# Optimization experiments

Measured on AMD Instinct MI355X. Metric: run time of the kernel, lower is better.

## Reference

```python
import jax, jax.numpy as jnp
import numpy as np

B, N, S, K, CIN = 16, 4096, 1024, 32, 64
EPS = 1e-5


def setup_inputs() -> dict:
    key = jax.random.key(0)
    ks = jax.random.split(key, 6)
    xyz = jax.random.normal(ks[0], (B, N, 3), jnp.float32)
    features = jax.random.normal(ks[1], (B, N, CIN), jnp.float32)
    # random sampling without replacement (mirrors torch.randperm(N)[:npoint])
    fps_idx = jax.vmap(lambda k: jax.random.permutation(k, N)[:S])(
        jax.random.split(ks[2], B)).astype(jnp.int32)
    chans = [CIN + 3, 64, 64, 128]
    params = {}
    for i in range(3):
        cin, cout = chans[i], chans[i + 1]
        params[f"W{i}"] = jax.random.normal(ks[3 + i], (cout, cin), jnp.float32) / np.sqrt(cin).astype(np.float32)
        params[f"b{i}"] = jnp.zeros((cout,), jnp.float32)
        params[f"g{i}"] = jnp.ones((cout,), jnp.float32)
        params[f"bt{i}"] = jnp.zeros((cout,), jnp.float32)
    return dict(xyz=xyz, features=features, fps_idx=fps_idx, **params)


def _mlp_layer(x, W, b, g, bt):
    # x: (B*S, Cin, K); Conv1d(kernel=1) + BatchNorm1d (training stats) + ReLU
    y = jnp.einsum('oc,bck->bok', W, x) + b[None, :, None]
    mu = y.mean(axis=(0, 2), keepdims=True)
    var = y.var(axis=(0, 2), keepdims=True)  # biased var, as in BN normalization
    y = (y - mu) * jax.lax.rsqrt(var + EPS) * g[None, :, None] + bt[None, :, None]
    return jax.nn.relu(y)


def reference(xyz, features, fps_idx, W0, b0, g0, bt0, W1, b1, g1, bt1, W2, b2, g2, bt2):
    # sample centers: (B, S, 3)
    new_xyz = jnp.take_along_axis(xyz, fps_idx[..., None], axis=1)
    # squared pairwise distances (B, S, N)
    d = (jnp.sum(new_xyz * new_xyz, -1)[..., None]
         + jnp.sum(xyz * xyz, -1)[:, None, :]
         - 2.0 * jnp.einsum('bsd,bnd->bsn', new_xyz, xyz))
    _, idx = jax.lax.top_k(-d, K)  # k nearest -> (B, S, K)
    bidx = jnp.arange(B)[:, None, None]
    g_xyz = xyz[bidx, idx] - new_xyz[:, :, None, :]  # (B, S, K, 3) relative coords
    g_feat = features[bidx, idx]                     # (B, S, K, CIN)
    grouped = jnp.concatenate([g_xyz, g_feat], axis=-1)  # (B, S, K, CIN+3)
    x = grouped.reshape(B * S, K, CIN + 3).transpose(0, 2, 1)  # (B*S, C, K)
    x = _mlp_layer(x, W0, b0, g0, bt0)
    x = _mlp_layer(x, W1, b1, g1, bt1)
    x = _mlp_layer(x, W2, b2, g2, bt2)
    new_features = x.max(axis=-1).reshape(B, S, -1)  # (B, S, 128)
    return new_xyz, new_features
```

## Files before the change

kernel.cpp:

```cpp
#include <hip/hip_runtime.h>
#include <stdint.h>

#define B_   16
#define N_   4096
#define S_   1024
#define K_   32
#define CIN_ 64
#define P_   524288
#define PQ_  16384
#define EPS_ 1e-5f

#define SZ_IDX    ((size_t)P_ * 4)
#define SZ_Y      ((size_t)P_ * 64 * 2)
#define SZ_MX     ((size_t)PQ_ * 128 * 4)
#define OFF_IDX   ((size_t)0)
#define OFF_Y0    (OFF_IDX + SZ_IDX)
#define OFF_Y1    (OFF_Y0 + SZ_Y)
#define OFF_MX    (OFF_Y1 + SZ_Y)
#define OFF_MN    (OFF_MX + SZ_MX)
#define OFF_STATS (OFF_MN + SZ_MX)
#define OFF_FIN   (OFF_STATS + 16384)
#define OFF_FPSC  (OFF_FIN + 2048)
#define OFF_PXYZW (OFF_FPSC + (size_t)PQ_ * 4)
#define WS_NEEDED (OFF_PXYZW + (size_t)B_ * N_ * 16)

typedef unsigned short u16;
typedef short bfrag __attribute__((ext_vector_type(8)));
typedef float f32x4 __attribute__((ext_vector_type(4)));

__device__ __forceinline__ float b2f(unsigned v) {
  return __uint_as_float((v & 0xffffu) << 16);
}
__device__ __forceinline__ u16 f2b(float f) {
  unsigned u = __float_as_uint(f);
  unsigned r = (u + 0x7fffu + ((u >> 16) & 1u)) >> 16;
  return (u16)r;
}
__device__ __forceinline__ unsigned pk2(float a, float b) {
  return (unsigned)f2b(a) | ((unsigned)f2b(b) << 16);
}

__global__ __launch_bounds__(256) void fps_canon_kernel(
    const int* __restrict__ fpsraw, int* __restrict__ fpsc)
{
  __shared__ int is64;
  const int tid = threadIdx.x;
  if (tid == 0) is64 = 1;
  __syncthreads();
  if (tid < 64) {
    if (fpsraw[2 * tid + 1] != 0) atomicAnd(&is64, 0);
  }
  __syncthreads();
  int i = blockIdx.x * 256 + tid;
  if (i < PQ_) {
    int src = is64 ? (2 * i) : i;
    int v = fpsraw[src];
    fpsc[i] = (v & 0xFFF);
  }
}

__global__ __launch_bounds__(256) void prep_kernel(
    const float* __restrict__ xyz, float4* __restrict__ pxyzw)
{
  int i = blockIdx.x * 256 + threadIdx.x;
  float x0 = xyz[i*3+0], x1 = xyz[i*3+1], x2 = xyz[i*3+2];
  float s2 = __fadd_rn(__fadd_rn(__fmul_rn(x0,x0), __fmul_rn(x1,x1)), __fmul_rn(x2,x2));
  pxyzw[i] = make_float4(x0, x1, x2, s2);
}

#define NBIN 2048
#define CAND_CAP 512

__global__ __launch_bounds__(256) void knn_kernel(
    const float4* __restrict__ pxyzw, const int* __restrict__ fps,
    int* __restrict__ idxout, float* __restrict__ out_xyz)
{
  __shared__ unsigned hist[NBIN];
  __shared__ float cd[CAND_CAP];
  __shared__ int   ci_[CAND_CAP];
  __shared__ int   sel[K_];
  __shared__ int   sCnt, sCand, sT;

  const int q   = blockIdx.x;
  const int b   = q >> 10;
  const int tid = threadIdx.x;
  const float4* xb4 = pxyzw + (size_t)b * N_;
  const int ctr = fps[q];
  const float4 cv = xb4[ctr];
  const float cx = cv.x, cy = cv.y, cz = cv.z, s1 = cv.w;

  if (tid == 0) {
    out_xyz[(size_t)q*3+0] = cx;
    out_xyz[(size_t)q*3+1] = cy;
    out_xyz[(size_t)q*3+2] = cz;
    sCnt = 0; sCand = 0;
  }
  {
    uint4* hz = (uint4*)hist;
    hz[tid]       = make_uint4(0,0,0,0);
    hz[tid + 256] = make_uint4(0,0,0,0);
  }
  __syncthreads();

  float dreg[16];
  unsigned bpk[8];
  #pragma unroll
  for (int it = 0; it < 16; ++it) {
    int n = it * 256 + tid;
    float4 v = xb4[n];
    float dt = __fadd_rn(__fadd_rn(__fmul_rn(cx,v.x), __fmul_rn(cy,v.y)), __fmul_rn(cz,v.z));
    float d  = __fsub_rn(__fadd_rn(s1, v.w), __fmul_rn(2.0f, dt));
    dreg[it] = d;
    int bin = (int)(d * 128.0f);
    bin = bin > (NBIN-1) ? (NBIN-1) : bin;
    bin = bin < 0 ? 0 : bin;
    if (it & 1) bpk[it >> 1] |= (unsigned)bin << 16;
    else        bpk[it >> 1]  = (unsigned)bin;
    atomicAdd(&hist[bin], 1u);
  }
  __syncthreads();

  const int lane = tid & 63, wid = tid >> 6;
  if (wid == 0) {
    int cum = 0, base = 0, found = 0;
    while (!found && base < NBIN) {
      int h = (int)hist[base + lane];
      int pre = h;
      #pragma unroll
      for (int off = 1; off < 64; off <<= 1) {
        int v = __shfl_up(pre, off, 64);
        if (lane >= off) pre += v;
      }
      int tot = __shfl(pre, 63, 64);
      bool cross = (cum + pre >= K_) && (cum + pre - h < K_);
      unsigned long long mm = __ballot(cross);
      if (mm) {
        if (lane == 0) sT = base + (int)(__ffsll((long long)mm) - 1);
        found = 1;
      }
      cum += tot;
      base += 64;
    }
  }
  __syncthreads();
  const int T = sT;

  #pragma unroll
  for (int it = 0; it < 16; ++it) {
    int bin = (int)((bpk[it >> 1] >> ((it & 1) * 16)) & 0xFFFFu);
    if (bin <= T) {
      int n = it * 256 + tid;
      if (bin < T) {
        int s = atomicAdd(&sCnt, 1);
        if (s < K_) sel[s] = n;
      } else {
        int s = atomicAdd(&sCand, 1);
        if (s < CAND_CAP) { cd[s] = dreg[it]; ci_[s] = n; }
      }
    }
  }
  __syncthreads();

  if (wid == 0) {
    int m = sCnt; m = m > K_ ? K_ : m;
    int cc = sCand; cc = cc > CAND_CAP ? CAND_CAP : cc;
    const int r = K_ - m;
    for (int it = 0; it < r; ++it) {
      float bd = 3.0e38f; int bi = 0x7fffffff;
      for (int j = lane; j < cc; j += 64) {
        float dv = cd[j]; int iv = ci_[j];
        if (dv < bd || (dv == bd && iv < bi)) { bd = dv; bi = iv; }
      }
      #pragma unroll
      for (int off = 32; off > 0; off >>= 1) {
        float od = __shfl_down(bd, off, 64);
        int   oi = __shfl_down(bi, off, 64);
        if (od < bd || (od == bd && oi < bi)) { bd = od; bi = oi; }
      }
      int win = __shfl(bi, 0, 64);
      if (lane == 0) sel[m + it] = win & 0xFFF;
      for (int j = lane; j < cc; j += 64) if (ci_[j] == win) cd[j] = 3.0e38f;
    }
  }
  __syncthreads();
  if (tid < K_) idxout[(size_t)q * K_ + tid] = sel[tid] & 0xFFF;
}


__global__ __launch_bounds__(256) void l0_mfma(
    const float* __restrict__ xyz, const float* __restrict__ feat,
    const int* __restrict__ fps, const int* __restrict__ idxin,
    const float* __restrict__ W0, const float* __restrict__ b0,
    uint4* __restrict__ Y0g, float* __restrict__ sumg, float* __restrict__ sqg)
{
  __shared__ uint4 Wl[12*64];
  __shared__ float bl[64];
  __shared__ float ssum[64], ssq[64];

  const int tid = threadIdx.x;
  const int bid0 = blockIdx.x;
  const int rep = (bid0 & 7) << 9;
  const int bid = (bid0 & 7) * ((int)gridDim.x >> 3) + (bid0 >> 3);
  const int pbase = bid * 128;
  const int q0 = bid * 4;
  const int b = bid >> 8;

  if (tid < 64) { bl[tid] = b0 ? b0[tid] : 0.f; ssum[tid] = 0.f; ssq[tid] = 0.f; }
  for (int u = tid; u < 12*64; u += 256) {
    int kc = u >> 6, o = u & 63;
    unsigned pk[4];
    #pragma unroll
    for (int hh = 0; hh < 4; ++hh) {
      int c0 = kc*8 + hh*2, c1 = c0 + 1;
      float v0 = (c0 < 64) ? W0[o*67 + 3 + c0] : (c0 < 67 ? W0[o*67 + (c0-64)] : 0.f);
      float v1 = (c1 < 64) ? W0[o*67 + 3 + c1] : (c1 < 67 ? W0[o*67 + (c1-64)] : 0.f);
      pk[hh] = pk2(v0, v1);
    }
    Wl[u] = make_uint4(pk[0], pk[1], pk[2], pk[3]);
  }

  const int lane = tid & 63, w = tid >> 6, g = lane >> 4, fr = lane & 15;
  const float* xb = xyz + (size_t)b * N_ * 3;
  const float* fbase = feat + (size_t)b * N_ * 64;

  int pidx[2];
  const int ct = fps[q0 + w] & 0xFFF;
  #pragma unroll
  for (int pm = 0; pm < 2; ++pm)
    pidx[pm] = idxin[pbase + w*32 + pm*16 + fr] & 0xFFF;

  bfrag xv[3][2];
  #pragma unroll
  for (int kk = 0; kk < 3; ++kk) {
    const int kc = kk*4 + g;
    #pragma unroll
    for (int pm = 0; pm < 2; ++pm) {
      uint4 uu;
      if (kc < 8) {
        const float* fp = fbase + pidx[pm]*64 + kc*8;
        float4 fa = *(const float4*)fp;
        float4 fb2 = *(const float4*)(fp + 4);
        uu = make_uint4(pk2(fa.x, fa.y), pk2(fa.z, fa.w),
                        pk2(fb2.x, fb2.y), pk2(fb2.z, fb2.w));
      } else if (kc == 8) {
        int n = pidx[pm];
        float dx = xb[n*3+0] - xb[ct*3+0];
        float dy = xb[n*3+1] - xb[ct*3+1];
        float dz = xb[n*3+2] - xb[ct*3+2];
        uu = make_uint4(pk2(dx, dy), (unsigned)f2b(dz), 0u, 0u);
      } else {
        uu = make_uint4(0u, 0u, 0u, 0u);
      }
      xv[kk][pm] = *(bfrag*)&uu;
    }
  }
  __syncthreads();

  f32x4 acc[4][2];
  #pragma unroll
  for (int m = 0; m < 4; ++m)
    #pragma unroll
    for (int j = 0; j < 4; ++j) {
      float v = bl[m*16 + g*4 + j];
      acc[m][0][j] = v; acc[m][1][j] = v;
    }
  #pragma unroll
  for (int kk = 0; kk < 3; ++kk) {
    const int kc = kk*4 + g;
    bfrag a[4];
    #pragma unroll
    for (int m = 0; m < 4; ++m) { uint4 u = Wl[kc*64 + m*16 + fr]; a[m] = *(bfrag*)&u; }
    #pragma unroll
    for (int m = 0; m < 4; ++m)
      #pragma unroll
      for (int pm = 0; pm < 2; ++pm)
        acc[m][pm] = __builtin_amdgcn_mfma_f32_16x16x32_bf16(a[m], xv[kk][pm], acc[m][pm], 0, 0, 0);
  }

  #pragma unroll
  for (int m = 0; m < 4; ++m) {
    #pragma unroll
    for (int j = 0; j < 4; ++j) {
      float v0 = acc[m][0][j], v1 = acc[m][1][j];
      float s = v0 + v1, s2 = v0*v0 + v1*v1;
      #pragma unroll
      for (int d = 1; d < 16; d <<= 1) { s += __shfl_xor(s, d); s2 += __shfl_xor(s2, d); }
      if (fr == 0) {
        atomicAdd(&ssum[m*16 + g*4 + j], s);
        atomicAdd(&ssq[m*16 + g*4 + j], s2);
      }
    }
    #pragma unroll
    for (int pm = 0; pm < 2; ++pm) {
      unsigned lo = pk2(acc[m][pm][0], acc[m][pm][1]);
      unsigned hi = pk2(acc[m][pm][2], acc[m][pm][3]);
      unsigned plo = (unsigned)__shfl_xor((int)lo, 16, 64);
      unsigned phi = (unsigned)__shfl_xor((int)hi, 16, 64);
      if ((g & 1) == 0) {
        size_t unit = (size_t)(m*2 + (g>>1)) * P_ + pbase + w*32 + pm*16 + fr;
        Y0g[unit] = make_uint4(lo, hi, plo, phi);
      }
    }
  }
  __syncthreads();
  if (tid < 64) { atomicAdd(&sumg[rep + tid], ssum[tid]); atomicAdd(&sqg[rep + tid], ssq[tid]); }
}

__global__ __launch_bounds__(256) void l1_mfma(
    const uint4* __restrict__ Y0g,
    const float* __restrict__ W1, const float* __restrict__ b1,
    const float* __restrict__ sc0, const float* __restrict__ sh0,
    uint4* __restrict__ Y1g, float* __restrict__ sumg, float* __restrict__ sqg)
{
  __shared__ uint4 Wl[8*64];
  __shared__ float scl[64], shl[64], bl[64];
  __shared__ float ssum[64], ssq[64];

  const int tid = threadIdx.x;
  const int bid0 = blockIdx.x;
  const int rep = (bid0 & 7) << 9;
  const int bid = (bid0 & 7) * ((int)gridDim.x >> 3) + (bid0 >> 3);
  const int pbase = bid * 128;

  if (tid < 64) {
    scl[tid] = sc0[tid]; shl[tid] = sh0[tid];
    bl[tid] = b1 ? b1[tid] : 0.f;
    ssum[tid] = 0.f; ssq[tid] = 0.f;
  }
  for (int u = tid; u < 8*64; u += 256) {
    int kc = u >> 6, o = u & 63;
    const float* wp = W1 + o*64 + kc*8;
    float4 wa = *(const float4*)wp;
    float4 wb = *(const float4*)(wp + 4);
    Wl[u] = make_uint4(pk2(wa.x, wa.y), pk2(wa.z, wa.w), pk2(wb.x, wb.y), pk2(wb.z, wb.w));
  }
  __syncthreads();

  const int lane = tid & 63, w = tid >> 6, g = lane >> 4, fr = lane & 15;

  bfrag xv[2][2];
  #pragma unroll
  for (int kk = 0; kk < 2; ++kk) {
    const int kc = kk*4 + g;
    float4 sa = *(const float4*)&scl[kc*8];
    float4 sb = *(const float4*)&scl[kc*8 + 4];
    float4 ha = *(const float4*)&shl[kc*8];
    float4 hb = *(const float4*)&shl[kc*8 + 4];
    #pragma unroll
    for (int pm = 0; pm < 2; ++pm) {
      uint4 yv = Y0g[(size_t)kc * P_ + pbase + w*32 + pm*16 + fr];
      unsigned r0 = pk2(fmaxf(fmaf(sa.x, b2f(yv.x),       ha.x), 0.f),
                        fmaxf(fmaf(sa.y, b2f(yv.x >> 16), ha.y), 0.f));
      unsigned r1 = pk2(fmaxf(fmaf(sa.z, b2f(yv.y),       ha.z), 0.f),
                        fmaxf(fmaf(sa.w, b2f(yv.y >> 16), ha.w), 0.f));
      unsigned r2 = pk2(fmaxf(fmaf(sb.x, b2f(yv.z),       hb.x), 0.f),
                        fmaxf(fmaf(sb.y, b2f(yv.z >> 16), hb.y), 0.f));
      unsigned r3 = pk2(fmaxf(fmaf(sb.z, b2f(yv.w),       hb.z), 0.f),
                        fmaxf(fmaf(sb.w, b2f(yv.w >> 16), hb.w), 0.f));
      uint4 uu = make_uint4(r0, r1, r2, r3);
      xv[kk][pm] = *(bfrag*)&uu;
    }
  }

  f32x4 acc[4][2];
  #pragma unroll
  for (int m = 0; m < 4; ++m)
    #pragma unroll
    for (int j = 0; j < 4; ++j) {
      float v = bl[m*16 + g*4 + j];
      acc[m][0][j] = v; acc[m][1][j] = v;
    }
  #pragma unroll
  for (int kk = 0; kk < 2; ++kk) {
    const int kc = kk*4 + g;
    bfrag a[4];
    #pragma unroll
    for (int m = 0; m < 4; ++m) { uint4 u = Wl[kc*64 + m*16 + fr]; a[m] = *(bfrag*)&u; }
    #pragma unroll
    for (int m = 0; m < 4; ++m)
      #pragma unroll
      for (int pm = 0; pm < 2; ++pm)
        acc[m][pm] = __builtin_amdgcn_mfma_f32_16x16x32_bf16(a[m], xv[kk][pm], acc[m][pm], 0, 0, 0);
  }

  #pragma unroll
  for (int m = 0; m < 4; ++m) {
    #pragma unroll
    for (int j = 0; j < 4; ++j) {
      float v0 = acc[m][0][j], v1 = acc[m][1][j];
      float s = v0 + v1, s2 = v0*v0 + v1*v1;
      #pragma unroll
      for (int d = 1; d < 16; d <<= 1) { s += __shfl_xor(s, d); s2 += __shfl_xor(s2, d); }
      if (fr == 0) {
        atomicAdd(&ssum[m*16 + g*4 + j], s);
        atomicAdd(&ssq[m*16 + g*4 + j], s2);
      }
    }
    #pragma unroll
    for (int pm = 0; pm < 2; ++pm) {
      unsigned lo = pk2(acc[m][pm][0], acc[m][pm][1]);
      unsigned hi = pk2(acc[m][pm][2], acc[m][pm][3]);
      unsigned plo = (unsigned)__shfl_xor((int)lo, 16, 64);
      unsigned phi = (unsigned)__shfl_xor((int)hi, 16, 64);
      if ((g & 1) == 0) {
        size_t unit = (size_t)(m*2 + (g>>1)) * P_ + pbase + w*32 + pm*16 + fr;
        Y1g[unit] = make_uint4(lo, hi, plo, phi);
      }
    }
  }
  __syncthreads();
  if (tid < 64) { atomicAdd(&sumg[rep + tid], ssum[tid]); atomicAdd(&sqg[rep + tid], ssq[tid]); }
}

__global__ __launch_bounds__(256) void l2_mfma(
    const uint4* __restrict__ Y1g,
    const float* __restrict__ W2, const float* __restrict__ b2,
    const float* __restrict__ sc1, const float* __restrict__ sh1,
    float* __restrict__ mxg, float* __restrict__ mng,
    float* __restrict__ sumg, float* __restrict__ sqg)
{
  __shared__ uint4 Wl[8*128];
  __shared__ float scl[64], shl[64], bl[128];
  __shared__ float ssum[128], ssq[128];

  const int tid = threadIdx.x;
  const int bid0 = blockIdx.x;
  const int rep = (bid0 & 7) << 9;
  const int bid = (bid0 & 7) * ((int)gridDim.x >> 3) + (bid0 >> 3);
  const int pbase = bid * 128;
  const int q0 = bid * 4;

  if (tid < 64) { scl[tid] = sc1[tid]; shl[tid] = sh1[tid]; }
  if (tid < 128) { bl[tid] = b2 ? b2[tid] : 0.f; ssum[tid] = 0.f; ssq[tid] = 0.f; }
  for (int u = tid; u < 8*128; u += 256) {
    int kc = u >> 7, o = u & 127;
    const float* wp = W2 + o*64 + kc*8;
    float4 wa = *(const float4*)wp;
    float4 wb = *(const float4*)(wp + 4);
    Wl[u] = make_uint4(pk2(wa.x, wa.y), pk2(wa.z, wa.w), pk2(wb.x, wb.y), pk2(wb.z, wb.w));
  }
  __syncthreads();

  const int lane = tid & 63, w = tid >> 6, g = lane >> 4, fr = lane & 15;

  bfrag ax[2][2];
  #pragma unroll
  for (int kk = 0; kk < 2; ++kk) {
    const int kc = kk*4 + g;
    float4 sa = *(const float4*)&scl[kc*8];
    float4 sb = *(const float4*)&scl[kc*8 + 4];
    float4 ha = *(const float4*)&shl[kc*8];
    float4 hb = *(const float4*)&shl[kc*8 + 4];
    #pragma unroll
    for (int pm = 0; pm < 2; ++pm) {
      uint4 yv = Y1g[(size_t)kc * P_ + pbase + w*32 + pm*16 + fr];
      unsigned r0 = pk2(fmaxf(fmaf(sa.x, b2f(yv.x),       ha.x), 0.f),
                        fmaxf(fmaf(sa.y, b2f(yv.x >> 16), ha.y), 0.f));
      unsigned r1 = pk2(fmaxf(fmaf(sa.z, b2f(yv.y),       ha.z), 0.f),
                        fmaxf(fmaf(sa.w, b2f(yv.y >> 16), ha.w), 0.f));
      unsigned r2 = pk2(fmaxf(fmaf(sb.x, b2f(yv.z),       hb.x), 0.f),
                        fmaxf(fmaf(sb.y, b2f(yv.z >> 16), hb.y), 0.f));
      unsigned r3 = pk2(fmaxf(fmaf(sb.z, b2f(yv.w),       hb.z), 0.f),
                        fmaxf(fmaf(sb.w, b2f(yv.w >> 16), hb.w), 0.f));
      uint4 uu = make_uint4(r0, r1, r2, r3);
      ax[kk][pm] = *(bfrag*)&uu;
    }
  }

  f32x4 acc[2][8];
  #pragma unroll
  for (int cn = 0; cn < 8; ++cn) {
    float v = bl[cn*16 + fr];
    #pragma unroll
    for (int j = 0; j < 4; ++j) { acc[0][cn][j] = v; acc[1][cn][j] = v; }
  }
  #pragma unroll
  for (int kk = 0; kk < 2; ++kk) {
    const int kc = kk*4 + g;
    #pragma unroll
    for (int cn = 0; cn < 8; ++cn) {
      uint4 u = Wl[kc*128 + cn*16 + fr];
      bfrag bw = *(bfrag*)&u;
      acc[0][cn] = __builtin_amdgcn_mfma_f32_16x16x32_bf16(ax[kk][0], bw, acc[0][cn], 0, 0, 0);
      acc[1][cn] = __builtin_amdgcn_mfma_f32_16x16x32_bf16(ax[kk][1], bw, acc[1][cn], 0, 0, 0);
    }
  }

  #pragma unroll
  for (int cn = 0; cn < 8; ++cn) {
    float mx = -3.0e38f, mn = 3.0e38f, s = 0.f, s2 = 0.f;
    #pragma unroll
    for (int pm = 0; pm < 2; ++pm)
      #pragma unroll
      for (int j = 0; j < 4; ++j) {
        float v = acc[pm][cn][j];
        mx = fmaxf(mx, v); mn = fminf(mn, v);
        s += v; s2 += v*v;
      }
    #pragma unroll
    for (int d = 16; d < 64; d <<= 1) {
      mx = fmaxf(mx, __shfl_xor(mx, d));
      mn = fminf(mn, __shfl_xor(mn, d));
      s  += __shfl_xor(s, d);
      s2 += __shfl_xor(s2, d);
    }
    if (g == 0) {
      int o = cn*16 + fr;
      size_t q = q0 + w;
      mxg[q*128 + o] = mx;
      mng[q*128 + o] = mn;
      atomicAdd(&ssum[o], s);
      atomicAdd(&ssq[o], s2);
    }
  }
  __syncthreads();
  if (tid < 128) { atomicAdd(&sumg[rep + tid], ssum[tid]); atomicAdd(&sqg[rep + tid], ssq[tid]); }
}

__global__ void finalize_kernel(
    const float* __restrict__ sum, const float* __restrict__ sq,
    const float* __restrict__ g, const float* __restrict__ bt,
    float* __restrict__ sc, float* __restrict__ sh, int C)
{
  int c = threadIdx.x;
  if (c < C) {
    float s = 0.f, s2 = 0.f;
    #pragma unroll
    for (int r = 0; r < 8; ++r) { s += sum[r*512 + c]; s2 += sq[r*512 + c]; }
    const float inv = 1.0f / (float)P_;
    float mu = s * inv;
    float var = s2 * inv - mu * mu;
    var = fmaxf(var, 0.f);
    float rr = 1.0f / sqrtf(var + EPS_);
    float gg = g ? g[c] : 1.0f;
    float bb = bt ? bt[c] : 0.0f;
    float sv = gg * rr;
    sc[c] = sv;
    sh[c] = bb - mu * sv;
  }
}

__global__ __launch_bounds__(256) void out_kernel(
    const float* __restrict__ mxg, const float* __restrict__ mng,
    const float* __restrict__ sc2, const float* __restrict__ sh2,
    float* __restrict__ out)
{
  int i = blockIdx.x * 256 + threadIdx.x;
  int o = i & 127;
  float a = sc2[o];
  float v = (a >= 0.f) ? mxg[i] : mng[i];
  float z = fmaxf(fmaf(a, v, sh2[o]), 0.f);
  out[(size_t)PQ_ * 3 + i] = z;
}

extern "C" void kernel_launch(void* const* d_in, const int* in_sizes, int n_in,
                              void* d_out, int out_size, void* d_ws, size_t ws_size,
                              hipStream_t stream)
{
  int i_xyz=-1, i_feat=-1, i_fps=-1, i_w0=-1, i_w1=-1, i_w2=-1;
  for (int i = 0; i < n_in; ++i) {
    switch (in_sizes[i]) {
      case 196608:  i_xyz = i; break;
      case 4194304: i_feat = i; break;
      case 16384:   i_fps = i; break;
      case 4288:    i_w0 = i; break;
      case 4096:    i_w1 = i; break;
      case 8192:    i_w2 = i; break;
      default: break;
    }
  }
  if (i_xyz < 0 || i_feat < 0 || i_fps < 0 || i_w0 < 0 || i_w1 < 0 || i_w2 < 0) return;

  const float* xyz  = (const float*)d_in[i_xyz];
  const float* feat = (const float*)d_in[i_feat];
  const int*   fpsr = (const int*)d_in[i_fps];
  const float* W0 = (const float*)d_in[i_w0];
  const float* W1 = (const float*)d_in[i_w1];
  const float* W2 = (const float*)d_in[i_w2];

  bool canon = (n_in >= 15 && i_xyz==0 && i_feat==1 && i_fps==2 && i_w0==3 &&
                i_w1==7 && i_w2==11 &&
                in_sizes[4]==64 && in_sizes[5]==64 && in_sizes[6]==64 &&
                in_sizes[8]==64 && in_sizes[9]==64 && in_sizes[10]==64 &&
                in_sizes[12]==128 && in_sizes[13]==128 && in_sizes[14]==128);
  const float* b0 = canon ? (const float*)d_in[4]  : nullptr;
  const float* g0 = canon ? (const float*)d_in[5]  : nullptr;
  const float* bt0= canon ? (const float*)d_in[6]  : nullptr;
  const float* b1 = canon ? (const float*)d_in[8]  : nullptr;
  const float* g1 = canon ? (const float*)d_in[9]  : nullptr;
  const float* bt1= canon ? (const float*)d_in[10] : nullptr;
  const float* b2 = canon ? (const float*)d_in[12] : nullptr;
  const float* g2 = canon ? (const float*)d_in[13] : nullptr;
  const float* bt2= canon ? (const float*)d_in[14] : nullptr;

  float* out = (float*)d_out;
  char* ws = (char*)d_ws;
  if (ws_size < WS_NEEDED) return;

  int* idxw = (int*)(ws + OFF_IDX);
  uint4* Y0 = (uint4*)(ws + OFF_Y0);
  uint4* Y1 = (uint4*)(ws + OFF_Y1);
  float* mxg = (float*)(ws + OFF_MX);
  float* mng = (float*)(ws + OFF_MN);
  float* st  = (float*)(ws + OFF_STATS);
  float* fin = (float*)(ws + OFF_FIN);
  int* fpsc  = (int*)(ws + OFF_FPSC);
  float4* pxyzw = (float4*)(ws + OFF_PXYZW);

  hipMemsetAsync(st, 0, 16384, stream);

  fps_canon_kernel<<<(PQ_+255)/256, 256, 0, stream>>>(fpsr, fpsc);
  prep_kernel<<<(B_*N_)/256, 256, 0, stream>>>(xyz, pxyzw);

  knn_kernel<<<PQ_, 256, 0, stream>>>(pxyzw, fpsc, idxw, out);

  l0_mfma<<<P_/128, 256, 0, stream>>>(xyz, feat, fpsc, idxw, W0, b0, Y0, st + 0, st + 64);
  finalize_kernel<<<1, 64, 0, stream>>>(st + 0, st + 64, g0, bt0, fin + 0, fin + 64, 64);

  l1_mfma<<<P_/128, 256, 0, stream>>>(Y0, W1, b1, fin + 0, fin + 64, Y1, st + 128, st + 192);
  finalize_kernel<<<1, 64, 0, stream>>>(st + 128, st + 192, g1, bt1, fin + 128, fin + 192, 64);

  l2_mfma<<<P_/128, 256, 0, stream>>>(Y1, W2, b2, fin + 128, fin + 192, mxg, mng, st + 256, st + 384);
  finalize_kernel<<<1, 128, 0, stream>>>(st + 256, st + 384, g2, bt2, fin + 256, fin + 384, 128);

  out_kernel<<<(PQ_*128)/256, 256, 0, stream>>>(mxg, mng, fin + 256, fin + 384, out);
}
```

Baseline: 238.4 us.

## Process two kNN queries per block with packed 16-bit histograms

Each kNN block now handles two query centers, so every loaded point coordinate is reused for two distance computations. The two histograms are packed as 16-bit halves of 32-bit words to keep shared memory the same size. Distances are recomputed for boundary candidates instead of being held in registers, and two wavefronts do the threshold scan and selection in parallel. The aim is to halve point loads and block count. The costs are more register pressure and possible atomic contention on the packed counters; a bin count over 65535 would overflow, though with 4096 points per query this cannot happen.

```diff
diff --git a/kernel.cpp b/kernel.cpp
--- a/kernel.cpp
+++ b/kernel.cpp
@@ -75,56 +75,62 @@
     const float4* __restrict__ pxyzw, const int* __restrict__ fps,
     int* __restrict__ idxout, float* __restrict__ out_xyz)
 {
-  __shared__ unsigned hist[NBIN];
-  __shared__ float cd[CAND_CAP];
-  __shared__ int   ci_[CAND_CAP];
-  __shared__ int   sel[K_];
-  __shared__ int   sCnt, sCand, sT;
-
-  const int q   = blockIdx.x;
-  const int b   = q >> 10;
+  __shared__ unsigned histp[2][NBIN/2];
+  __shared__ float cd[2][CAND_CAP];
+  __shared__ int   ci_[2][CAND_CAP];
+  __shared__ int   sel[2][K_];
+  __shared__ int   sCnt[2], sCand[2], sT[2];
+
+  const int q0  = blockIdx.x * 2;
+  const int b   = q0 >> 10;
   const int tid = threadIdx.x;
   const float4* xb4 = pxyzw + (size_t)b * N_;
-  const int ctr = fps[q];
-  const float4 cv = xb4[ctr];
-  const float cx = cv.x, cy = cv.y, cz = cv.z, s1 = cv.w;
-
-  if (tid == 0) {
-    out_xyz[(size_t)q*3+0] = cx;
-    out_xyz[(size_t)q*3+1] = cy;
-    out_xyz[(size_t)q*3+2] = cz;
-    sCnt = 0; sCand = 0;
+  const int ctr0 = fps[q0]     & 0xFFF;
+  const int ctr1 = fps[q0 + 1] & 0xFFF;
+  const float4 c0 = xb4[ctr0];
+  const float4 c1 = xb4[ctr1];
+
+  if (tid < 2) {
+    const float4 cc = tid ? c1 : c0;
+    out_xyz[(size_t)(q0 + tid)*3+0] = cc.x;
+    out_xyz[(size_t)(q0 + tid)*3+1] = cc.y;
+    out_xyz[(size_t)(q0 + tid)*3+2] = cc.z;
+    sCnt[tid] = 0; sCand[tid] = 0;
   }
   {
-    uint4* hz = (uint4*)hist;
-    hz[tid]       = make_uint4(0,0,0,0);
+    uint4* hz = (uint4*)&histp[0][0];
+    hz[tid] = make_uint4(0,0,0,0);
     hz[tid + 256] = make_uint4(0,0,0,0);
   }
   __syncthreads();
 
-  float dreg[16];
-  unsigned bpk[8];
+  unsigned bpk0[8], bpk1[8];
   #pragma unroll
   for (int it = 0; it < 16; ++it) {
     int n = it * 256 + tid;
     float4 v = xb4[n];
-    float dt = __fadd_rn(__fadd_rn(__fmul_rn(cx,v.x), __fmul_rn(cy,v.y)), __fmul_rn(cz,v.z));
-    float d  = __fsub_rn(__fadd_rn(s1, v.w), __fmul_rn(2.0f, dt));
-    dreg[it] = d;
-    int bin = (int)(d * 128.0f);
-    bin = bin > (NBIN-1) ? (NBIN-1) : bin;
-    bin = bin < 0 ? 0 : bin;
-    if (it & 1) bpk[it >> 1] |= (unsigned)bin << 16;
-    else        bpk[it >> 1]  = (unsigned)bin;
-    atomicAdd(&hist[bin], 1u);
+    float dt0 = __fadd_rn(__fadd_rn(__fmul_rn(c0.x,v.x), __fmul_rn(c0.y,v.y)), __fmul_rn(c0.z,v.z));
+    float d0  = __fsub_rn(__fadd_rn(c0.w, v.w), __fmul_rn(2.0f, dt0));
+    float dt1 = __fadd_rn(__fadd_rn(__fmul_rn(c1.x,v.x), __fmul_rn(c1.y,v.y)), __fmul_rn(c1.z,v.z));
+    float d1  = __fsub_rn(__fadd_rn(c1.w, v.w), __fmul_rn(2.0f, dt1));
+    int b0 = (int)(d0 * 128.0f);
+    b0 = b0 > (NBIN-1) ? (NBIN-1) : b0; b0 = b0 < 0 ? 0 : b0;
+    int b1 = (int)(d1 * 128.0f);
+    b1 = b1 > (NBIN-1) ? (NBIN-1) : b1; b1 = b1 < 0 ? 0 : b1;
+    if (it & 1) { bpk0[it >> 1] |= (unsigned)b0 << 16; bpk1[it >> 1] |= (unsigned)b1 << 16; }
+    else        { bpk0[it >> 1]  = (unsigned)b0;       bpk1[it >> 1]  = (unsigned)b1; }
+    atomicAdd(&histp[0][b0 >> 1], (b0 & 1) ? 0x10000u : 1u);
+    atomicAdd(&histp[1][b1 >> 1], (b1 & 1) ? 0x10000u : 1u);
   }
   __syncthreads();
 
   const int lane = tid & 63, wid = tid >> 6;
-  if (wid == 0) {
+  if (wid < 2) {
+    const unsigned* hq = &histp[wid][0];
     int cum = 0, base = 0, found = 0;
     while (!found && base < NBIN) {
-      int h = (int)hist[base + lane];
+      int bn = base + lane;
+      int h = (int)((hq[bn >> 1] >> ((bn & 1) * 16)) & 0xFFFFu);
       int pre = h;
       #pragma unroll
       for (int off = 1; off < 64; off <<= 1) {
@@ -135,7 +141,7 @@
       bool cross = (cum + pre >= K_) && (cum + pre - h < K_);
       unsigned long long mm = __ballot(cross);
       if (mm) {
-        if (lane == 0) sT = base + (int)(__ffsll((long long)mm) - 1);
+        if (lane == 0) sT[wid] = base + (int)(__ffsll((long long)mm) - 1);
         found = 1;
       }
       cum += tot;
@@ -143,32 +149,55 @@
     }
   }
   __syncthreads();
-  const int T = sT;
+  const int T0 = sT[0], T1 = sT[1];
 
   #pragma unroll
   for (int it = 0; it < 16; ++it) {
-    int bin = (int)((bpk[it >> 1] >> ((it & 1) * 16)) & 0xFFFFu);
-    if (bin <= T) {
+    int b0 = (int)((bpk0[it >> 1] >> ((it & 1) * 16)) & 0xFFFFu);
+    if (b0 <= T0) {
       int n = it * 256 + tid;
-      if (bin < T) {
-        int s = atomicAdd(&sCnt, 1);
-        if (s < K_) sel[s] = n;
+      if (b0 < T0) {
+        int s = atomicAdd(&sCnt[0], 1);
+        if (s < K_) sel[0][s] = n;
       } else {
-        int s = atomicAdd(&sCand, 1);
-        if (s < CAND_CAP) { cd[s] = dreg[it]; ci_[s] = n; }
-      }
-    }
-  }
-  __syncthreads();
-
-  if (wid == 0) {
-    int m = sCnt; m = m > K_ ? K_ : m;
-    int cc = sCand; cc = cc > CAND_CAP ? CAND_CAP : cc;
+        int s = atomicAdd(&sCand[0], 1);
+        if (s < CAND_CAP) {
+          float4 v = xb4[n];
+          float dt = __fadd_rn(__fadd_rn(__fmul_rn(c0.x,v.x), __fmul_rn(c0.y,v.y)), __fmul_rn(c0.z,v.z));
+          float d  = __fsub_rn(__fadd_rn(c0.w, v.w), __fmul_rn(2.0f, dt));
+          cd[0][s] = d; ci_[0][s] = n;
+        }
+      }
+    }
+    int b1 = (int)((bpk1[it >> 1] >> ((it & 1) * 16)) & 0xFFFFu);
+    if (b1 <= T1) {
+      int n = it * 256 + tid;
+      if (b1 < T1) {
+        int s = atomicAdd(&sCnt[1], 1);
+        if (s < K_) sel[1][s] = n;
+      } else {
+        int s = atomicAdd(&sCand[1], 1);
+        if (s < CAND_CAP) {
+          float4 v = xb4[n];
+          float dt = __fadd_rn(__fadd_rn(__fmul_rn(c1.x,v.x), __fmul_rn(c1.y,v.y)), __fmul_rn(c1.z,v.z));
+          float d  = __fsub_rn(__fadd_rn(c1.w, v.w), __fmul_rn(2.0f, dt));
+          cd[1][s] = d; ci_[1][s] = n;
+        }
+      }
+    }
+  }
+  __syncthreads();
+
+  if (wid < 2) {
+    int m = sCnt[wid]; m = m > K_ ? K_ : m;
+    int cc = sCand[wid]; cc = cc > CAND_CAP ? CAND_CAP : cc;
     const int r = K_ - m;
+    float* cdq = &cd[wid][0];
+    int* ciq = &ci_[wid][0];
     for (int it = 0; it < r; ++it) {
       float bd = 3.0e38f; int bi = 0x7fffffff;
       for (int j = lane; j < cc; j += 64) {
-        float dv = cd[j]; int iv = ci_[j];
+        float dv = cdq[j]; int iv = ciq[j];
         if (dv < bd || (dv == bd && iv < bi)) { bd = dv; bi = iv; }
       }
       #pragma unroll
@@ -178,12 +207,15 @@
         if (od < bd || (od == bd && oi < bi)) { bd = od; bi = oi; }
       }
       int win = __shfl(bi, 0, 64);
-      if (lane == 0) sel[m + it] = win & 0xFFF;
-      for (int j = lane; j < cc; j += 64) if (ci_[j] == win) cd[j] = 3.0e38f;
-    }
-  }
-  __syncthreads();
-  if (tid < K_) idxout[(size_t)q * K_ + tid] = sel[tid] & 0xFFF;
+      if (lane == 0) sel[wid][m + it] = win & 0xFFF;
+      for (int j = lane; j < cc; j += 64) if (ciq[j] == win) cdq[j] = 3.0e38f;
+    }
+  }
+  __syncthreads();
+  if (tid < 2 * K_) {
+    int qq = tid >> 5, kk = tid & 31;
+    idxout[(size_t)(q0 + qq) * K_ + kk] = sel[qq][kk] & 0xFFF;
+  }
 }
 
 
@@ -612,7 +644,7 @@
   fps_canon_kernel<<<(PQ_+255)/256, 256, 0, stream>>>(fpsr, fpsc);
   prep_kernel<<<(B_*N_)/256, 256, 0, stream>>>(xyz, pxyzw);
 
-  knn_kernel<<<PQ_, 256, 0, stream>>>(pxyzw, fpsc, idxw, out);
+  knn_kernel<<<PQ_/2, 256, 0, stream>>>(pxyzw, fpsc, idxw, out);
 
   l0_mfma<<<P_/128, 256, 0, stream>>>(xyz, feat, fpsc, idxw, W0, b0, Y0, st + 0, st + 64);
   finalize_kernel<<<1, 64, 0, stream>>>(st + 0, st + 64, g0, bt0, fin + 0, fin + 64, 64);
```

New measurement: 242.7 us. No clear change (+1.8%).
